# Performance work log

Hardware: AMD Instinct MI355X
Metric: run time of the kernel (lower is better)

## Reference

```python
import jax, jax.numpy as jnp
import numpy as np

H = 128
T = 120
F_IN = 180
BN_EPS = 1e-5
LEAKY_SLOPE = 0.01


def _lstm_layer(x, wih, whh, bih, bhh):
    """Single LSTM layer. x: (B,T,D); wih:(4H,D), whh:(4H,H). PyTorch gate order i,f,g,o."""
    B = x.shape[0]
    # Precompute input projections for all timesteps: (B,T,4H)
    x_proj = jnp.einsum('btd,gd->btg', x, wih) + bih + bhh
    x_proj = jnp.transpose(x_proj, (1, 0, 2))  # (T,B,4H) for scan over time
    h0 = jnp.zeros((B, H), dtype=x.dtype)
    c0 = jnp.zeros((B, H), dtype=x.dtype)

    def step(carry, xt):
        h, c = carry
        gates = xt + h @ whh.T  # (B,4H)
        i, f, g, o = jnp.split(gates, 4, axis=-1)
        i = jax.nn.sigmoid(i)
        f = jax.nn.sigmoid(f)
        g = jnp.tanh(g)
        o = jax.nn.sigmoid(o)
        c = f * c + i * g
        h = o * jnp.tanh(c)
        return (h, c), h

    (_, _), hs = jax.lax.scan(step, (h0, c0), x_proj)  # hs: (T,B,H)
    return jnp.transpose(hs, (1, 0, 2))  # (B,T,H)


def setup_inputs() -> dict:
    key = jax.random.key(0)
    ks = jax.random.split(key, 16)
    B = 2048
    s = 0.1  # keep activations in a stable range
    inp = {
        'x': jax.random.normal(ks[0], (B, F_IN, T), jnp.float32),
        'fc_w': jax.random.normal(ks[1], (H, F_IN), jnp.float32) * s,
        'fc_b': jax.random.normal(ks[2], (H,), jnp.float32) * s,
        'bn_g': jax.random.uniform(ks[3], (H,), jnp.float32, 0.5, 1.5),
        'bn_b': jax.random.normal(ks[4], (H,), jnp.float32) * s,
        'bn_mean': jax.random.normal(ks[5], (H,), jnp.float32) * s,
        'bn_var': jax.random.uniform(ks[6], (H,), jnp.float32, 0.5, 1.5),
        'wih0': jax.random.normal(ks[7], (4 * H, H), jnp.float32) * s,
        'whh0': jax.random.normal(ks[8], (4 * H, H), jnp.float32) * s,
        'bih0': jax.random.normal(ks[9], (4 * H,), jnp.float32) * s,
        'bhh0': jax.random.normal(ks[10], (4 * H,), jnp.float32) * s,
        'wih1': jax.random.normal(ks[11], (4 * H, H), jnp.float32) * s,
        'whh1': jax.random.normal(ks[12], (4 * H, H), jnp.float32) * s,
        'bih1': jax.random.normal(ks[13], (4 * H,), jnp.float32) * s,
        'bhh1': jax.random.normal(ks[14], (4 * H,), jnp.float32) * s,
    }
    return inp


def reference(x, fc_w, fc_b, bn_g, bn_b, bn_mean, bn_var,
              wih0, whh0, bih0, bhh0, wih1, whh1, bih1, bhh1):
    # x.reshape(-1,180,120).permute(0,2,1) -> (B,120,180)
    h = jnp.transpose(x.reshape(-1, F_IN, T), (0, 2, 1)).reshape(-1, F_IN)
    # Linear + BatchNorm1d (eval mode) + LeakyReLU
    h = h @ fc_w.T + fc_b
    h = (h - bn_mean) * jax.lax.rsqrt(bn_var + BN_EPS) * bn_g + bn_b
    h = jnp.where(h >= 0, h, LEAKY_SLOPE * h)
    h = h.reshape(-1, T, H)
    # 2-layer LSTM, take last timestep
    h = _lstm_layer(h, wih0, whh0, bih0, bhh0)
    h = _lstm_layer(h, wih1, whh1, bih1, bhh1)
    return h[:, -1, :]
```

## Files before the change

### kernel.cpp

```cpp
#include <hip/hip_runtime.h>

#define T_STEPS 120
#define NF_IN   180
#define H_DIM   128
#define G_DIM   512
#define K_FC    192
#define HP      136
#define XP_TILE 4096

typedef __attribute__((ext_vector_type(8))) short short8;
typedef __attribute__((ext_vector_type(4))) float f32x4;

__device__ __forceinline__ f32x4 mfma16(short8 a, short8 b, f32x4 c) {
    return __builtin_amdgcn_mfma_f32_16x16x32_bf16(a, b, c, 0, 0, 0);
}

__device__ __forceinline__ short f2bf(float x) {
    union { float f; unsigned u; } v; v.f = x;
    unsigned r = v.u + 0x7fffu + ((v.u >> 16) & 1u);
    return (short)(r >> 16);
}

__device__ __forceinline__ float sigm(float x) {
    return __builtin_amdgcn_rcpf(1.f + __expf(-x));
}
__device__ __forceinline__ float tanh_f(float x) {
    return 1.f - 2.f * __builtin_amdgcn_rcpf(1.f + __expf(2.f * x));
}

__global__ void prep_kernel(
    const float* __restrict__ fc_w, const float* __restrict__ fc_b,
    const float* __restrict__ bn_g, const float* __restrict__ bn_b,
    const float* __restrict__ bn_mean, const float* __restrict__ bn_var,
    const float* __restrict__ wih0, const float* __restrict__ whh0,
    const float* __restrict__ bih0, const float* __restrict__ bhh0,
    const float* __restrict__ wih1, const float* __restrict__ whh1,
    const float* __restrict__ bih1, const float* __restrict__ bhh1,
    short* __restrict__ fcw_o, float* __restrict__ fcb_o,
    float* __restrict__ bias0_o, float* __restrict__ bias1_o,
    short* __restrict__ wih0_o, short* __restrict__ whh0_o,
    short* __restrict__ wih1_o, short* __restrict__ whh1_o)
{
    int tid = blockIdx.x * blockDim.x + threadIdx.x;
    int stride = gridDim.x * blockDim.x;
    for (int i = tid; i < H_DIM * K_FC; i += stride) {
        int h = i / K_FC, f = i % K_FC;
        float s = bn_g[h] * rsqrtf(bn_var[h] + 1e-5f);
        float v = (f < NF_IN) ? fc_w[h * NF_IN + f] * s : 0.f;
        fcw_o[i] = f2bf(v);
    }
    for (int i = tid; i < H_DIM; i += stride) {
        float s = bn_g[i] * rsqrtf(bn_var[i] + 1e-5f);
        fcb_o[i] = (fc_b[i] - bn_mean[i]) * s + bn_b[i];
    }
    for (int i = tid; i < G_DIM; i += stride) {
        bias0_o[i] = bih0[i] + bhh0[i];
        bias1_o[i] = bih1[i] + bhh1[i];
    }
    for (int i = tid; i < G_DIM * H_DIM; i += stride) {
        wih0_o[i] = f2bf(wih0[i]); whh0_o[i] = f2bf(whh0[i]);
        wih1_o[i] = f2bf(wih1[i]); whh1_o[i] = f2bf(whh1[i]);
    }
}

__global__ __launch_bounds__(256) void fc_kernel(
    const float* __restrict__ x, const short* __restrict__ fcw,
    const float* __restrict__ fcb, short* __restrict__ xfc)
{
    __shared__ short outs[120 * 132];
    const int b = blockIdx.x;
    const int tid = threadIdx.x;
    const int wave = tid >> 6, lane = tid & 63;
    const int m16 = lane & 15, q = lane >> 4;

    short8 af[2][6];
#pragma unroll
    for (int mi = 0; mi < 2; ++mi) {
        int t = (wave * 2 + mi) * 16 + m16;
        if (t > 119) t = 119;
        const float* xb = x + (size_t)b * (NF_IN * T_STEPS) + (size_t)q * 8 * T_STEPS + t;
#pragma unroll
        for (int kc = 0; kc < 6; ++kc) {
            union { short s[8]; short8 v; } u;
#pragma unroll
            for (int j = 0; j < 8; ++j) {
                int f = kc * 32 + q * 8 + j;
                float val = (f < NF_IN) ? xb[(kc * 32 + j) * T_STEPS] : 0.f;
                u.s[j] = f2bf(val);
            }
            af[mi][kc] = u.v;
        }
    }

    float fcb_v[8];
#pragma unroll
    for (int nt = 0; nt < 8; ++nt) fcb_v[nt] = fcb[nt * 16 + m16];

    f32x4 acc[2][8];
#pragma unroll
    for (int mi = 0; mi < 2; ++mi)
#pragma unroll
        for (int nt = 0; nt < 8; ++nt) acc[mi][nt] = (f32x4){0.f, 0.f, 0.f, 0.f};

#pragma unroll
    for (int nt = 0; nt < 8; ++nt) {
        short8 bf[6];
#pragma unroll
        for (int kc = 0; kc < 6; ++kc)
            bf[kc] = *(const short8*)(fcw + (nt * 16 + m16) * K_FC + kc * 32 + q * 8);
#pragma unroll
        for (int mi = 0; mi < 2; ++mi)
#pragma unroll
            for (int kc = 0; kc < 6; ++kc)
                acc[mi][nt] = mfma16(af[mi][kc], bf[kc], acc[mi][nt]);
    }

#pragma unroll
    for (int mi = 0; mi < 2; ++mi)
#pragma unroll
        for (int nt = 0; nt < 8; ++nt)
#pragma unroll
            for (int r = 0; r < 4; ++r) {
                int t = (wave * 2 + mi) * 16 + q * 4 + r;
                int h = nt * 16 + m16;
                float v = acc[mi][nt][r] + fcb_v[nt];
                v = (v >= 0.f) ? v : 0.01f * v;
                if (t < 120) outs[t * 132 + h] = f2bf(v);
            }
    __syncthreads();

    unsigned* dst = (unsigned*)xfc + (size_t)b * (T_STEPS * H_DIM / 2);
    const unsigned* srcs = (const unsigned*)outs;
    for (int i = tid; i < T_STEPS * H_DIM / 2; i += 256) {
        int t = i >> 6, c2 = i & 63;
        dst[i] = srcs[t * 66 + c2];
    }
}

__global__ __launch_bounds__(512, 2) void lstm_kernel(
    const short* h_in,
    const short* __restrict__ wih,
    const short* __restrict__ whh,
    const float* __restrict__ bias,
    short* h_out,
    float* __restrict__ fout)
{
    __shared__ short h_lds[2 * 8 * HP];
    __shared__ float xp_lds[2 * XP_TILE];

    const int tid = threadIdx.x;
    const int wave = tid >> 6, lane = tid & 63;
    const int q = lane >> 4, m16 = lane & 15, m8 = m16 & 7;
    const int qv = q & 1;
    const int b0 = blockIdx.x * 8;
    const bool cons = wave < 4;
    const int d = wave & 3;

    for (int i = tid; i < 8 * HP; i += 512) ((unsigned*)h_lds)[i] = 0u;

    const short* W = cons ? whh : wih;
    short8 wf[4][2][4];
    float bias_v[4][2];
#pragma unroll
    for (int g = 0; g < 4; ++g)
#pragma unroll
        for (int j = 0; j < 2; ++j) {
            int n = g * 128 + d * 32 + j * 16 + m16;
            bias_v[g][j] = bias[n];
#pragma unroll
            for (int kc = 0; kc < 4; ++kc)
                wf[g][j][kc] = *(const short8*)(W + n * H_DIM + kc * 32 + q * 8);
        }

    float c[2][4];
#pragma unroll
    for (int j = 0; j < 2; ++j)
#pragma unroll
        for (int r = 0; r < 4; ++r) c[j][r] = 0.f;

    auto prod = [&](int t) {
        const short* src = h_in + ((size_t)(b0 + m8) * T_STEPS + t) * H_DIM + q * 8;
        short8 ax[4];
#pragma unroll
        for (int kc = 0; kc < 4; ++kc) ax[kc] = *(const short8*)(src + kc * 32);
        float* xpb = xp_lds + (t & 1) * XP_TILE;
#pragma unroll
        for (int g = 0; g < 4; ++g)
#pragma unroll
            for (int j = 0; j < 2; ++j) {
                float bv = bias_v[g][j];
                f32x4 acc = (f32x4){bv, bv, bv, bv};
#pragma unroll
                for (int kc = 0; kc < 4; ++kc) acc = mfma16(ax[kc], wf[g][j][kc], acc);
                if (q < 2)
                    *(f32x4*)(xpb + ((d * 8 + g * 2 + j) * 16 + m16) * 8 + q * 4) = acc;
            }
    };

    if (!cons) prod(0);
    __syncthreads();

    for (int s = 0; s < T_STEPS; ++s) {
        if (cons) {
            const short* hb = h_lds + ((s + 1) & 1) * (8 * HP) + m8 * HP + q * 8;
            short8 ar[4];
#pragma unroll
            for (int kc = 0; kc < 4; ++kc) ar[kc] = *(const short8*)(hb + kc * 32);
            f32x4 racc[4][2];
#pragma unroll
            for (int g = 0; g < 4; ++g)
#pragma unroll
                for (int j = 0; j < 2; ++j) {
                    f32x4 acc = (f32x4){0.f, 0.f, 0.f, 0.f};
#pragma unroll
                    for (int kc = 0; kc < 4; ++kc) acc = mfma16(ar[kc], wf[g][j][kc], acc);
                    racc[g][j] = acc;
                }
            const float* xpb = xp_lds + (s & 1) * XP_TILE;
            short* hw = h_lds + (s & 1) * (8 * HP);
#pragma unroll
            for (int j = 0; j < 2; ++j) {
                f32x4 xv[4];
#pragma unroll
                for (int g = 0; g < 4; ++g)
                    xv[g] = *(const f32x4*)(xpb + ((d * 8 + g * 2 + j) * 16 + m16) * 8 + qv * 4);
#pragma unroll
                for (int r = 0; r < 4; ++r) {
                    float iv = sigm(racc[0][j][r] + xv[0][r]);
                    float fv = sigm(racc[1][j][r] + xv[1][r]);
                    float gv = tanh_f(racc[2][j][r] + xv[2][r]);
                    float ov = sigm(racc[3][j][r] + xv[3][r]);
                    float cc = fv * c[j][r] + iv * gv;
                    c[j][r] = cc;
                    float hv = ov * tanh_f(cc);
                    if (q < 2) {
                        hw[(q * 4 + r) * HP + d * 32 + j * 16 + m16] = f2bf(hv);
                        if (fout != nullptr && s == T_STEPS - 1)
                            fout[(size_t)(b0 + q * 4 + r) * H_DIM + d * 32 + j * 16 + m16] = hv;
                    }
                }
            }
        } else {
            if (s + 1 < T_STEPS) prod(s + 1);
        }
        if (h_out != nullptr && s >= 1) {
            int row = tid >> 6, c2 = tid & 63;
            unsigned v = ((const unsigned*)h_lds)[((s + 1) & 1) * (4 * HP) + row * (HP / 2) + c2];
            ((unsigned*)h_out)[((size_t)(b0 + row) * T_STEPS + (s - 1)) * (H_DIM / 2) + c2] = v;
        }
        __syncthreads();
    }
    if (h_out != nullptr) {
        int row = tid >> 6, c2 = tid & 63;
        unsigned v = ((const unsigned*)h_lds)[1 * (4 * HP) + row * (HP / 2) + c2];
        ((unsigned*)h_out)[((size_t)(b0 + row) * T_STEPS + (T_STEPS - 1)) * (H_DIM / 2) + c2] = v;
    }
}

static constexpr size_t OFF_FCW  = 0;
static constexpr size_t OFF_FCB  = 49152;
static constexpr size_t OFF_B0   = 49664;
static constexpr size_t OFF_B1   = 51712;
static constexpr size_t OFF_WIH0 = 53760;
static constexpr size_t OFF_WHH0 = 184832;
static constexpr size_t OFF_WIH1 = 315904;
static constexpr size_t OFF_WHH1 = 446976;
static constexpr size_t OFF_BUFA = 578048;

extern "C" void kernel_launch(void* const* d_in, const int* in_sizes, int n_in,
                              void* d_out, int out_size, void* d_ws, size_t ws_size,
                              hipStream_t stream) {
    const float* x       = (const float*)d_in[0];
    const float* fc_w    = (const float*)d_in[1];
    const float* fc_b    = (const float*)d_in[2];
    const float* bn_g    = (const float*)d_in[3];
    const float* bn_b    = (const float*)d_in[4];
    const float* bn_mean = (const float*)d_in[5];
    const float* bn_var  = (const float*)d_in[6];
    const float* wih0    = (const float*)d_in[7];
    const float* whh0    = (const float*)d_in[8];
    const float* bih0    = (const float*)d_in[9];
    const float* bhh0    = (const float*)d_in[10];
    const float* wih1    = (const float*)d_in[11];
    const float* whh1    = (const float*)d_in[12];
    const float* bih1    = (const float*)d_in[13];
    const float* bhh1    = (const float*)d_in[14];

    const int B = in_sizes[0] / (NF_IN * T_STEPS);

    char* ws = (char*)d_ws;
    short* fcw   = (short*)(ws + OFF_FCW);
    float* fcb   = (float*)(ws + OFF_FCB);
    float* bias0 = (float*)(ws + OFF_B0);
    float* bias1 = (float*)(ws + OFF_B1);
    short* wih0b = (short*)(ws + OFF_WIH0);
    short* whh0b = (short*)(ws + OFF_WHH0);
    short* wih1b = (short*)(ws + OFF_WIH1);
    short* whh1b = (short*)(ws + OFF_WHH1);
    short* bufA  = (short*)(ws + OFF_BUFA);

    prep_kernel<<<256, 256, 0, stream>>>(
        fc_w, fc_b, bn_g, bn_b, bn_mean, bn_var,
        wih0, whh0, bih0, bhh0, wih1, whh1, bih1, bhh1,
        fcw, fcb, bias0, bias1, wih0b, whh0b, wih1b, whh1b);

    fc_kernel<<<B, 256, 0, stream>>>(x, fcw, fcb, bufA);

    lstm_kernel<<<B / 8, 512, 0, stream>>>(bufA, wih0b, whh0b, bias0, bufA, nullptr);
    lstm_kernel<<<B / 8, 512, 0, stream>>>(bufA, wih1b, whh1b, bias1, nullptr, (float*)d_out);
}
```

Measured before the change: 654.6 us.

## Split LSTM work across all eight waves and fold gate scaling into weights

The LSTM kernel drops the producer/consumer wave split, where four waves did the recurrent matmul and four did the input projection. Now all eight waves each handle a 16-column gate slice of both matmuls. Recurrent results are staged through a new LDS buffer so every lane does the activation math for two elements instead of eight. The weights and biases are pre-scaled by -1 (sigmoid gates) or 2 (tanh gate) in the prep kernel, which removes the negate and multiply before each exp. The cost is an extra LDS round trip for the recurrent accumulators and more weight registers per wave.

```diff
diff --git a/kernel.cpp b/kernel.cpp
--- a/kernel.cpp
+++ b/kernel.cpp
@@ -6,7 +6,7 @@
 #define G_DIM   512
 #define K_FC    192
 #define HP      136
-#define XP_TILE 4096
+#define XPR     12
 
 typedef __attribute__((ext_vector_type(8))) short short8;
 typedef __attribute__((ext_vector_type(4))) float f32x4;
@@ -21,11 +21,11 @@
     return (short)(r >> 16);
 }
 
-__device__ __forceinline__ float sigm(float x) {
-    return __builtin_amdgcn_rcpf(1.f + __expf(-x));
-}
-__device__ __forceinline__ float tanh_f(float x) {
-    return 1.f - 2.f * __builtin_amdgcn_rcpf(1.f + __expf(2.f * x));
+__device__ __forceinline__ float sig_y(float y) {
+    return __builtin_amdgcn_rcpf(1.f + __expf(y));
+}
+__device__ __forceinline__ float tanh_y(float y) {
+    return 1.f - 2.f * __builtin_amdgcn_rcpf(1.f + __expf(y));
 }
 
 __global__ void prep_kernel(
@@ -54,12 +54,14 @@
         fcb_o[i] = (fc_b[i] - bn_mean[i]) * s + bn_b[i];
     }
     for (int i = tid; i < G_DIM; i += stride) {
-        bias0_o[i] = bih0[i] + bhh0[i];
-        bias1_o[i] = bih1[i] + bhh1[i];
+        float sc = ((i >> 7) == 2) ? 2.f : -1.f;
+        bias0_o[i] = (bih0[i] + bhh0[i]) * sc;
+        bias1_o[i] = (bih1[i] + bhh1[i]) * sc;
     }
     for (int i = tid; i < G_DIM * H_DIM; i += stride) {
-        wih0_o[i] = f2bf(wih0[i]); whh0_o[i] = f2bf(whh0[i]);
-        wih1_o[i] = f2bf(wih1[i]); whh1_o[i] = f2bf(whh1[i]);
+        float sc = ((i >> 7) / H_DIM == 2) ? 2.f : -1.f;
+        wih0_o[i] = f2bf(wih0[i] * sc); whh0_o[i] = f2bf(whh0[i] * sc);
+        wih1_o[i] = f2bf(wih1[i] * sc); whh1_o[i] = f2bf(whh1[i] * sc);
     }
 }
 
@@ -146,103 +148,106 @@
     float* __restrict__ fout)
 {
     __shared__ short h_lds[2 * 8 * HP];
-    __shared__ float xp_lds[2 * XP_TILE];
+    __shared__ float xp_lds[2 * G_DIM * XPR];
+    __shared__ float rc_lds[G_DIM * XPR];
 
     const int tid = threadIdx.x;
-    const int wave = tid >> 6, lane = tid & 63;
-    const int q = lane >> 4, m16 = lane & 15, m8 = m16 & 7;
-    const int qv = q & 1;
+    const int w = tid >> 6, lane = tid & 63;
+    const int m16 = lane & 15, q = lane >> 4, m8 = m16 & 7;
+    const int dl = m16, rp = q;
     const int b0 = blockIdx.x * 8;
-    const bool cons = wave < 4;
-    const int d = wave & 3;
 
     for (int i = tid; i < 8 * HP; i += 512) ((unsigned*)h_lds)[i] = 0u;
 
-    const short* W = cons ? whh : wih;
-    short8 wf[4][2][4];
-    float bias_v[4][2];
-#pragma unroll
-    for (int g = 0; g < 4; ++g)
-#pragma unroll
-        for (int j = 0; j < 2; ++j) {
-            int n = g * 128 + d * 32 + j * 16 + m16;
-            bias_v[g][j] = bias[n];
-#pragma unroll
-            for (int kc = 0; kc < 4; ++kc)
-                wf[g][j][kc] = *(const short8*)(W + n * H_DIM + kc * 32 + q * 8);
-        }
-
-    float c[2][4];
-#pragma unroll
-    for (int j = 0; j < 2; ++j)
-#pragma unroll
-        for (int r = 0; r < 4; ++r) c[j][r] = 0.f;
-
-    auto prod = [&](int t) {
+    short8 whf[4][4], wif[4][4];
+    float bias_v[4];
+#pragma unroll
+    for (int g = 0; g < 4; ++g) {
+        int n = g * 128 + w * 16 + m16;
+        bias_v[g] = bias[n];
+#pragma unroll
+        for (int kc = 0; kc < 4; ++kc) {
+            whf[g][kc] = *(const short8*)(whh + n * H_DIM + kc * 32 + q * 8);
+            wif[g][kc] = *(const short8*)(wih + n * H_DIM + kc * 32 + q * 8);
+        }
+    }
+
+    float c0 = 0.f, c1 = 0.f;
+
+    auto loadA = [&](short8 ax[4], int t) {
         const short* src = h_in + ((size_t)(b0 + m8) * T_STEPS + t) * H_DIM + q * 8;
+#pragma unroll
+        for (int kc = 0; kc < 4; ++kc) ax[kc] = *(const short8*)(src + kc * 32);
+    };
+    auto prodMFMA = [&](short8 ax[4], int t) {
+        float* xpb = xp_lds + (t & 1) * (G_DIM * XPR);
+#pragma unroll
+        for (int g = 0; g < 4; ++g) {
+            float bv = bias_v[g];
+            f32x4 acc = (f32x4){bv, bv, bv, bv};
+#pragma unroll
+            for (int kc = 0; kc < 4; ++kc) acc = mfma16(ax[kc], wif[g][kc], acc);
+            if (q < 2)
+                *(f32x4*)(xpb + (g * 128 + w * 16 + m16) * XPR + q * 4) = acc;
+        }
+    };
+
+    {
         short8 ax[4];
-#pragma unroll
-        for (int kc = 0; kc < 4; ++kc) ax[kc] = *(const short8*)(src + kc * 32);
-        float* xpb = xp_lds + (t & 1) * XP_TILE;
-#pragma unroll
-        for (int g = 0; g < 4; ++g)
-#pragma unroll
-            for (int j = 0; j < 2; ++j) {
-                float bv = bias_v[g][j];
-                f32x4 acc = (f32x4){bv, bv, bv, bv};
-#pragma unroll
-                for (int kc = 0; kc < 4; ++kc) acc = mfma16(ax[kc], wf[g][j][kc], acc);
-                if (q < 2)
-                    *(f32x4*)(xpb + ((d * 8 + g * 2 + j) * 16 + m16) * 8 + q * 4) = acc;
-            }
-    };
-
-    if (!cons) prod(0);
+        loadA(ax, 0);
+        prodMFMA(ax, 0);
+    }
     __syncthreads();
 
     for (int s = 0; s < T_STEPS; ++s) {
-        if (cons) {
+        short8 ax[4];
+        if (s + 1 < T_STEPS) loadA(ax, s + 1);
+
+        {
             const short* hb = h_lds + ((s + 1) & 1) * (8 * HP) + m8 * HP + q * 8;
             short8 ar[4];
 #pragma unroll
             for (int kc = 0; kc < 4; ++kc) ar[kc] = *(const short8*)(hb + kc * 32);
-            f32x4 racc[4][2];
-#pragma unroll
-            for (int g = 0; g < 4; ++g)
-#pragma unroll
-                for (int j = 0; j < 2; ++j) {
-                    f32x4 acc = (f32x4){0.f, 0.f, 0.f, 0.f};
-#pragma unroll
-                    for (int kc = 0; kc < 4; ++kc) acc = mfma16(ar[kc], wf[g][j][kc], acc);
-                    racc[g][j] = acc;
-                }
-            const float* xpb = xp_lds + (s & 1) * XP_TILE;
+#pragma unroll
+            for (int g = 0; g < 4; ++g) {
+                f32x4 acc = (f32x4){0.f, 0.f, 0.f, 0.f};
+#pragma unroll
+                for (int kc = 0; kc < 4; ++kc) acc = mfma16(ar[kc], whf[g][kc], acc);
+                if (q < 2)
+                    *(f32x4*)(rc_lds + (g * 128 + w * 16 + m16) * XPR + q * 4) = acc;
+            }
+        }
+
+        if (s + 1 < T_STEPS) prodMFMA(ax, s + 1);
+
+        {
+            const float* xpb = xp_lds + (s & 1) * (G_DIM * XPR);
+            float2 rd[4], xd[4];
+#pragma unroll
+            for (int g = 0; g < 4; ++g) {
+                int n = (g * 128 + w * 16 + dl) * XPR + rp * 2;
+                rd[g] = *(const float2*)(rc_lds + n);
+                xd[g] = *(const float2*)(xpb + n);
+            }
+            float i0 = sig_y(rd[0].x + xd[0].x), i1 = sig_y(rd[0].y + xd[0].y);
+            float f0 = sig_y(rd[1].x + xd[1].x), f1 = sig_y(rd[1].y + xd[1].y);
+            float g0 = tanh_y(rd[2].x + xd[2].x), g1 = tanh_y(rd[2].y + xd[2].y);
+            float o0 = sig_y(rd[3].x + xd[3].x), o1 = sig_y(rd[3].y + xd[3].y);
+            c0 = f0 * c0 + i0 * g0;
+            c1 = f1 * c1 + i1 * g1;
+            float h0v = o0 * tanh_y(2.f * c0);
+            float h1v = o1 * tanh_y(2.f * c1);
+
             short* hw = h_lds + (s & 1) * (8 * HP);
-#pragma unroll
-            for (int j = 0; j < 2; ++j) {
-                f32x4 xv[4];
-#pragma unroll
-                for (int g = 0; g < 4; ++g)
-                    xv[g] = *(const f32x4*)(xpb + ((d * 8 + g * 2 + j) * 16 + m16) * 8 + qv * 4);
-#pragma unroll
-                for (int r = 0; r < 4; ++r) {
-                    float iv = sigm(racc[0][j][r] + xv[0][r]);
-                    float fv = sigm(racc[1][j][r] + xv[1][r]);
-                    float gv = tanh_f(racc[2][j][r] + xv[2][r]);
-                    float ov = sigm(racc[3][j][r] + xv[3][r]);
-                    float cc = fv * c[j][r] + iv * gv;
-                    c[j][r] = cc;
-                    float hv = ov * tanh_f(cc);
-                    if (q < 2) {
-                        hw[(q * 4 + r) * HP + d * 32 + j * 16 + m16] = f2bf(hv);
-                        if (fout != nullptr && s == T_STEPS - 1)
-                            fout[(size_t)(b0 + q * 4 + r) * H_DIM + d * 32 + j * 16 + m16] = hv;
-                    }
-                }
-            }
-        } else {
-            if (s + 1 < T_STEPS) prod(s + 1);
-        }
+            int dim = w * 16 + dl;
+            hw[(rp * 2) * HP + dim]     = f2bf(h0v);
+            hw[(rp * 2 + 1) * HP + dim] = f2bf(h1v);
+            if (fout != nullptr && s == T_STEPS - 1) {
+                fout[(size_t)(b0 + rp * 2) * H_DIM + dim]     = h0v;
+                fout[(size_t)(b0 + rp * 2 + 1) * H_DIM + dim] = h1v;
+            }
+        }
+
         if (h_out != nullptr && s >= 1) {
             int row = tid >> 6, c2 = tid & 63;
             unsigned v = ((const unsigned*)h_lds)[((s + 1) & 1) * (4 * HP) + row * (HP / 2) + c2];
```

Result: slower. 730.1 us (+11.5%).
